# Kernel optimization log

Hardware: AMD Instinct MI355X
Metric: run time of the kernel (lower is better)

Reference implementation:

```python
import jax, jax.numpy as jnp
import numpy as np

B = 4096
INPUT_DIM = 4096
N_BLOCKS = 8
BLOCK = INPUT_DIM // N_BLOCKS  # 512
N_EXPERTS = 6
H = 1024   # expert_hidden
H2 = H // 2


def setup_inputs() -> dict:
    key = jax.random.key(0)
    ks = jax.random.split(key, 16)
    s = 0.02  # init scale keeps tanh/softmax in sane range
    return {
        "x":   jax.random.normal(ks[0], (B, INPUT_DIM), jnp.float32),
        # routers: per-block stacked weights [8, ...]
        "Wr1": jax.random.normal(ks[1], (N_BLOCKS, BLOCK, 32), jnp.float32) * s,
        "br1": jax.random.normal(ks[2], (N_BLOCKS, 32), jnp.float32) * s,
        "Wr2": jax.random.normal(ks[3], (N_BLOCKS, 32, N_EXPERTS), jnp.float32) * s,
        "br2": jax.random.normal(ks[4], (N_BLOCKS, N_EXPERTS), jnp.float32) * s,
        # experts: stacked [6, ...], shared across all 8 blocks
        "We1": jax.random.normal(ks[5], (N_EXPERTS, BLOCK, H), jnp.float32) * s,
        "be1": jax.random.normal(ks[6], (N_EXPERTS, H), jnp.float32) * s,
        "We2": jax.random.normal(ks[7], (N_EXPERTS, H, H2), jnp.float32) * s,
        "be2": jax.random.normal(ks[8], (N_EXPERTS, H2), jnp.float32) * s,
        "We3": jax.random.normal(ks[9], (N_EXPERTS, H2, 3), jnp.float32) * s,
        "be3": jax.random.normal(ks[10], (N_EXPERTS, 3), jnp.float32) * s,
        # aggregator
        "Wa1": jax.random.normal(ks[11], (3, 16), jnp.float32) * s,
        "ba1": jax.random.normal(ks[12], (16,), jnp.float32) * s,
        "Wa2": jax.random.normal(ks[13], (16, 3), jnp.float32) * s,
        "ba2": jax.random.normal(ks[14], (3,), jnp.float32) * s,
    }


def reference(x, Wr1, br1, Wr2, br2, We1, be1, We2, be2, We3, be3,
              Wa1, ba1, Wa2, ba2):
    b = x.shape[0]
    blocks = x.reshape(b, N_BLOCKS, BLOCK)                       # [b,s,d]
    # routers (one per block s)
    r1 = jax.nn.relu(jnp.einsum('bsd,sdh->bsh', blocks, Wr1) + br1)
    routing = jax.nn.softmax(
        jnp.einsum('bsh,she->bse', r1, Wr2) + br2, axis=-1)      # [b,s,E]
    # experts applied to every block (grouped GEMMs)
    h1 = jnp.tanh(jnp.einsum('bsd,edh->bseh', blocks, We1) + be1)        # [b,s,E,H]
    h2 = jnp.tanh(jnp.einsum('bseh,ehk->bsek', h1, We2) + be2)           # [b,s,E,H2]
    eo = jnp.einsum('bsek,eko->bseo', h2, We3) + be3                     # [b,s,E,3]
    weighted = jnp.einsum('bse,bseo->bso', routing, eo)                  # [b,s,3]
    final = weighted.mean(axis=1)                                        # mean over 8 blocks
    a1 = jax.nn.relu(final @ Wa1 + ba1)
    return a1 @ Wa2 + ba2                                                # [b,3]
```

## Files before the change

### kernel.cpp

```cpp
#include <hip/hip_runtime.h>
#include <cstdint>
#include <cstddef>

typedef __bf16 bf16;
typedef __bf16 bf16x4 __attribute__((ext_vector_type(4)));
typedef __bf16 bf16x8 __attribute__((ext_vector_type(8)));
typedef float  f32x4  __attribute__((ext_vector_type(4)));
typedef long long i64v;

#define NROWS   32768
#define DBLK    512
#define H1N     1024
#define H2N     512
#define NEXP    6
#define NBATCH  4096
#define HALL    (NEXP * H1N)
#define W2SCALE 32.0f
#define W2INV   0.03125f

__device__ __forceinline__ void gld16(const void* g, void* l) {
    __builtin_amdgcn_global_load_lds(
        (const __attribute__((address_space(1))) void*)g,
        (__attribute__((address_space(3))) void*)l, 16, 0, 0);
}

__device__ __forceinline__ float fast_tanh(float x) {
    float e = __expf(2.0f * x);
    return 1.0f - __fdividef(2.0f, e + 1.0f);
}

__device__ __forceinline__ float hsum16(float v) {
    v += __shfl_xor(v, 1);
    v += __shfl_xor(v, 2);
    v += __shfl_xor(v, 4);
    v += __shfl_xor(v, 8);
    return v;
}

__device__ __forceinline__ int swz(int row, int g) {
    return row * 64 + ((g ^ (row & 7)) * 8);
}
__device__ __forceinline__ int swz8(int row, int g) {
    return row * 64 + ((g ^ ((row >> 1) & 3)) << 4);
}


__global__ void cvt_bf16_kernel(const float* __restrict__ in,
                                bf16* __restrict__ out, int n4) {
    int i = blockIdx.x * blockDim.x + threadIdx.x;
    if (i >= n4) return;
    float4 v = ((const float4*)in)[i];
    bf16x4 o;
    o.x = (bf16)v.x; o.y = (bf16)v.y; o.z = (bf16)v.z; o.w = (bf16)v.w;
    ((bf16x4*)out)[i] = o;
}

__global__ __launch_bounds__(256) void transpose_cvt(
    const float* __restrict__ in, bf16* __restrict__ out, int K, int N) {
    __shared__ bf16 tile[64][66];
    int e  = blockIdx.z;
    int n0 = blockIdx.x * 64;
    int k0 = blockIdx.y * 64;
    int c  = threadIdx.x & 63;
    int rb = threadIdx.x >> 6;
    const float* src = in + (size_t)e * K * N;
    bf16* dst = out + (size_t)e * N * K;
#pragma unroll
    for (int it = 0; it < 16; ++it) {
        int k = k0 + rb + it * 4;
        int n = n0 + c;
        if (k < K && n < N) tile[rb + it * 4][c] = (bf16)src[(size_t)k * N + n];
    }
    __syncthreads();
#pragma unroll
    for (int it = 0; it < 16; ++it) {
        int n = n0 + rb + it * 4;
        int k = k0 + c;
        if (n < N && k < K) dst[(size_t)n * K + k] = tile[c][rb + it * 4];
    }
}

__global__ __launch_bounds__(256) void transpose_cvt_fp8(
    const float* __restrict__ in, uint8_t* __restrict__ out, int K, int N,
    float scale) {
    __shared__ float tile[64][65];
    int e  = blockIdx.z;
    int n0 = blockIdx.x * 64;
    int k0 = blockIdx.y * 64;
    int c  = threadIdx.x & 63;
    int rb = threadIdx.x >> 6;
    const float* src = in + (size_t)e * K * N;
    uint8_t* dst = out + (size_t)e * N * K;
#pragma unroll
    for (int it = 0; it < 16; ++it) {
        int k = k0 + rb + it * 4;
        int n = n0 + c;
        if (k < K && n < N) tile[rb + it * 4][c] = src[(size_t)k * N + n];
    }
    __syncthreads();
#pragma unroll
    for (int it = 0; it < 16; ++it) {
        int n = n0 + rb + it * 4;
        int k = k0 + c;
        if (n < N && k < K) {
            float v = tile[c][rb + it * 4] * scale;
            int p = __builtin_amdgcn_cvt_pk_fp8_f32(v, v, 0, false);
            dst[(size_t)n * K + k] = (uint8_t)(p & 0xff);
        }
    }
}

__global__ void zero_f32_kernel(float* __restrict__ p, int n) {
    int i = blockIdx.x * blockDim.x + threadIdx.x;
    if (i < n) p[i] = 0.0f;
}


__global__ __launch_bounds__(256, 2) void router_kernel(
    const bf16* __restrict__ xbf,
    const bf16* __restrict__ Wr1t,
    const float* __restrict__ br1,
    const float* __restrict__ Wr2,
    const float* __restrict__ br2,
    float* __restrict__ routing) {
    __shared__ __align__(16) bf16 sA[128 * 64];
    __shared__ __align__(16) bf16 sB[32 * 64];
    const int tid = threadIdx.x;
    const int w = tid >> 6, l = tid & 63;
    const int s  = blockIdx.y;
    const int b0 = blockIdx.x * 128;
    const int wm = w * 32;
    const int srow = l >> 3, schk = (l & 7) * 8;
    const int fr = l & 15, fq = l >> 4;
    const bf16* Ab = xbf + (size_t)s * 512;
    const bf16* Bb = Wr1t + (size_t)s * (32 * 512);

    f32x4 acc[2][2];
#pragma unroll
    for (int i = 0; i < 2; ++i)
#pragma unroll
        for (int j = 0; j < 2; ++j) acc[i][j] = (f32x4){0.f, 0.f, 0.f, 0.f};

    for (int k0 = 0; k0 < 512; k0 += 64) {
        __syncthreads();
#pragma unroll
        for (int jj = 0; jj < 4; ++jj) {
            int row = w * 32 + jj * 8;
            gld16(Ab + (size_t)(b0 + row + srow) * 4096 + k0 + schk, sA + row * 64);
        }
        gld16(Bb + (size_t)(w * 8 + srow) * 512 + k0 + schk, sB + w * 8 * 64);
        __syncthreads();
#pragma unroll
        for (int ks = 0; ks < 2; ++ks) {
            bf16x8 af[2], bfr[2];
#pragma unroll
            for (int i = 0; i < 2; ++i)
                af[i] = *(const bf16x8*)&sA[(wm + i * 16 + fr) * 64 + ks * 32 + fq * 8];
#pragma unroll
            for (int j = 0; j < 2; ++j)
                bfr[j] = *(const bf16x8*)&sB[(j * 16 + fr) * 64 + ks * 32 + fq * 8];
#pragma unroll
            for (int i = 0; i < 2; ++i)
#pragma unroll
                for (int j = 0; j < 2; ++j)
                    acc[i][j] = __builtin_amdgcn_mfma_f32_16x16x32_bf16(
                        af[i], bfr[j], acc[i][j], 0, 0, 0);
        }
    }

    float b1v[2], w2v[2][6], br2v[6];
#pragma unroll
    for (int j = 0; j < 2; ++j) {
        int col = j * 16 + fr;
        b1v[j] = br1[s * 32 + col];
#pragma unroll
        for (int e2 = 0; e2 < 6; ++e2) w2v[j][e2] = Wr2[(s * 32 + col) * 6 + e2];
    }
#pragma unroll
    for (int e2 = 0; e2 < 6; ++e2) br2v[e2] = br2[s * 6 + e2];

#pragma unroll
    for (int i = 0; i < 2; ++i) {
#pragma unroll
        for (int r = 0; r < 4; ++r) {
            float lg[6] = {0.f, 0.f, 0.f, 0.f, 0.f, 0.f};
#pragma unroll
            for (int j = 0; j < 2; ++j) {
                float t = fmaxf(acc[i][j][r] + b1v[j], 0.f);
#pragma unroll
                for (int e2 = 0; e2 < 6; ++e2) lg[e2] += t * w2v[j][e2];
            }
#pragma unroll
            for (int e2 = 0; e2 < 6; ++e2) lg[e2] = hsum16(lg[e2]) + br2v[e2];
            float mx = lg[0];
#pragma unroll
            for (int e2 = 1; e2 < 6; ++e2) mx = fmaxf(mx, lg[e2]);
            float p[6], sum = 0.f;
#pragma unroll
            for (int e2 = 0; e2 < 6; ++e2) { p[e2] = __expf(lg[e2] - mx); sum += p[e2]; }
            float inv = __fdividef(1.f, sum);
            if (fr == 0) {
                int brow = b0 + wm + i * 16 + fq * 4 + r;
                float* dst = routing + ((size_t)brow * 8 + s) * 6;
#pragma unroll
                for (int e2 = 0; e2 < 6; ++e2) dst[e2] = p[e2] * inv;
            }
        }
    }
}

__global__ __launch_bounds__(256, 4) void gemm1_kernel(
    const bf16* __restrict__ A,
    const bf16* __restrict__ B,
    const float* __restrict__ bias,
    uint8_t* __restrict__ h1,
    int ldh) {
    __shared__ __align__(16) bf16 sA[128 * 64];
    __shared__ __align__(16) bf16 sB[128 * 64];
    const int tid = threadIdx.x;
    const int w = tid >> 6, l = tid & 63;
    const int n0 = blockIdx.x * 128;
    const int m0 = blockIdx.y * 128;
    const int wm = (w & 1) * 64, wn = (w >> 1) * 64;
    const int srow = l >> 3;
    const int gcol = ((l & 7) ^ srow) * 8;
    const int fr = l & 15, fq = l >> 4;

    f32x4 acc[4][4];
#pragma unroll
    for (int i = 0; i < 4; ++i)
#pragma unroll
        for (int j = 0; j < 4; ++j) acc[i][j] = (f32x4){0.f, 0.f, 0.f, 0.f};

    for (int k0 = 0; k0 < DBLK; k0 += 64) {
        __syncthreads();
#pragma unroll
        for (int jj = 0; jj < 4; ++jj) {
            int row = w * 32 + jj * 8;
            gld16(A + (size_t)(m0 + row + srow) * DBLK + k0 + gcol, sA + row * 64);
            gld16(B + (size_t)(n0 + row + srow) * DBLK + k0 + gcol, sB + row * 64);
        }
        __syncthreads();
#pragma unroll
        for (int ks = 0; ks < 2; ++ks) {
            bf16x8 af[4], bfr[4];
#pragma unroll
            for (int i = 0; i < 4; ++i)
                af[i] = *(const bf16x8*)&sA[swz(wm + i * 16 + fr, ks * 4 + fq)];
#pragma unroll
            for (int j = 0; j < 4; ++j)
                bfr[j] = *(const bf16x8*)&sB[swz(wn + j * 16 + fr, ks * 4 + fq)];
#pragma unroll
            for (int i = 0; i < 4; ++i)
#pragma unroll
                for (int j = 0; j < 4; ++j)
                    acc[i][j] = __builtin_amdgcn_mfma_f32_16x16x32_bf16(
                        af[i], bfr[j], acc[i][j], 0, 0, 0);
        }
    }

#pragma unroll
    for (int i = 0; i < 4; ++i) {
        int colb = m0 + wm + i * 16 + fq * 4;
        float4 bb = *(const float4*)&bias[colb];
#pragma unroll
        for (int j = 0; j < 4; ++j) {
            int xrow = n0 + wn + j * 16 + fr;
            float t0 = fast_tanh(acc[i][j][0] + bb.x);
            float t1 = fast_tanh(acc[i][j][1] + bb.y);
            float t2 = fast_tanh(acc[i][j][2] + bb.z);
            float t3 = fast_tanh(acc[i][j][3] + bb.w);
            int p = 0;
            p = __builtin_amdgcn_cvt_pk_fp8_f32(t0, t1, p, false);
            p = __builtin_amdgcn_cvt_pk_fp8_f32(t2, t3, p, true);
            *(uint32_t*)&h1[(size_t)xrow * ldh + colb] = (uint32_t)p;
        }
    }
}

__global__ __launch_bounds__(256, 4) void gemm2_kernel(
    const uint8_t* __restrict__ h1,
    const uint8_t* __restrict__ W2f8t,
    const float* __restrict__ be2,
    const float* __restrict__ We3,
    float* __restrict__ eo,
    int ldh) {
    __shared__ __align__(16) uint8_t sA[128 * 64];
    __shared__ __align__(16) uint8_t sB[128 * 64];
    __shared__ float w3s[128 * 3];
    __shared__ float b2s[128];
    const int tid = threadIdx.x;
    const int w = tid >> 6, l = tid & 63;
    const int e  = blockIdx.z;
    const int n0 = blockIdx.x * 128;
    const int m0 = blockIdx.y * 128;
    const int wm = (w & 1) * 64, wn = (w >> 1) * 64;
    const int srow4 = l >> 2;
    const int g4 = (((l & 3) ^ ((l >> 3) & 3)) << 4);
    const int fr = l & 15, fq = l >> 4;
    const uint8_t* Ae = W2f8t + (size_t)e * (H2N * H1N);
    const uint8_t* Be = h1 + (size_t)e * H1N;

    if (tid < 128) {
        int c = m0 + tid;
        b2s[tid] = be2[e * H2N + c];
        w3s[tid * 3 + 0] = We3[((size_t)e * H2N + c) * 3 + 0];
        w3s[tid * 3 + 1] = We3[((size_t)e * H2N + c) * 3 + 1];
        w3s[tid * 3 + 2] = We3[((size_t)e * H2N + c) * 3 + 2];
    }

    f32x4 acc[4][4];
#pragma unroll
    for (int i = 0; i < 4; ++i)
#pragma unroll
        for (int j = 0; j < 4; ++j) acc[i][j] = (f32x4){0.f, 0.f, 0.f, 0.f};

    for (int k0 = 0; k0 < H1N; k0 += 64) {
        __syncthreads();
#pragma unroll
        for (int jj = 0; jj < 2; ++jj) {
            int row = w * 32 + jj * 16 + srow4;
            gld16(Ae + (size_t)(m0 + row) * H1N + k0 + g4, sA + (w * 32 + jj * 16) * 64);
            gld16(Be + (size_t)(n0 + row) * ldh + k0 + g4, sB + (w * 32 + jj * 16) * 64);
        }
        __syncthreads();
#pragma unroll
        for (int ks = 0; ks < 2; ++ks) {
            i64v af[4], bfr[4];
#pragma unroll
            for (int i = 0; i < 4; ++i) {
                int row = wm + i * 16 + fr;
                af[i] = *(const i64v*)&sA[swz8(row, ks * 2 + (fq >> 1)) + ((fq & 1) << 3)];
            }
#pragma unroll
            for (int j = 0; j < 4; ++j) {
                int row = wn + j * 16 + fr;
                bfr[j] = *(const i64v*)&sB[swz8(row, ks * 2 + (fq >> 1)) + ((fq & 1) << 3)];
            }
#pragma unroll
            for (int i = 0; i < 4; ++i)
#pragma unroll
                for (int j = 0; j < 4; ++j)
                    acc[i][j] = __builtin_amdgcn_mfma_f32_16x16x32_fp8_fp8(
                        af[i], bfr[j], acc[i][j], 0, 0, 0);
        }
    }

    float p[4][3];
#pragma unroll
    for (int j = 0; j < 4; ++j) { p[j][0] = 0.f; p[j][1] = 0.f; p[j][2] = 0.f; }
#pragma unroll
    for (int i = 0; i < 4; ++i) {
        int cl = wm + i * 16 + fq * 4;
        float4 bb = *(const float4*)&b2s[cl];
        float4 wa = *(const float4*)&w3s[cl * 3 + 0];
        float4 wb = *(const float4*)&w3s[cl * 3 + 4];
        float4 wc = *(const float4*)&w3s[cl * 3 + 8];
        float bias4[4] = {bb.x, bb.y, bb.z, bb.w};
        float w30[4] = {wa.x, wa.w, wb.z, wc.y};
        float w31[4] = {wa.y, wb.x, wb.w, wc.z};
        float w32[4] = {wa.z, wb.y, wc.x, wc.w};
#pragma unroll
        for (int j = 0; j < 4; ++j) {
#pragma unroll
            for (int r = 0; r < 4; ++r) {
                float t = fast_tanh(acc[i][j][r] * W2INV + bias4[r]);
                p[j][0] += t * w30[r];
                p[j][1] += t * w31[r];
                p[j][2] += t * w32[r];
            }
        }
    }
#pragma unroll
    for (int j = 0; j < 4; ++j) {
        float v0 = p[j][0], v1 = p[j][1], v2 = p[j][2];
        v0 += __shfl_xor(v0, 16); v0 += __shfl_xor(v0, 32);
        v1 += __shfl_xor(v1, 16); v1 += __shfl_xor(v1, 32);
        v2 += __shfl_xor(v2, 16); v2 += __shfl_xor(v2, 32);
        if (fq == 0) {
            int xrow = n0 + wn + j * 16 + fr;
            float* dst = eo + ((size_t)e * NROWS + xrow) * 3;
            atomicAdd(dst + 0, v0);
            atomicAdd(dst + 1, v1);
            atomicAdd(dst + 2, v2);
        }
    }
}

__global__ void final_kernel(
    const float* __restrict__ routing, const float* __restrict__ eo,
    const float* __restrict__ be3, const float* __restrict__ Wa1,
    const float* __restrict__ ba1, const float* __restrict__ Wa2,
    const float* __restrict__ ba2, float* __restrict__ out) {
    int b = blockIdx.x * blockDim.x + threadIdx.x;
    if (b >= NBATCH) return;
    float f0 = 0.f, f1 = 0.f, f2 = 0.f;
    for (int s = 0; s < 8; ++s) {
        int r = b * 8 + s;
        const float* rt = routing + (size_t)r * 6;
#pragma unroll
        for (int e = 0; e < 6; ++e) {
            float wgt = rt[e];
            const float* eop = eo + ((size_t)e * NROWS + r) * 3;
            f0 += wgt * (eop[0] + be3[e * 3 + 0]);
            f1 += wgt * (eop[1] + be3[e * 3 + 1]);
            f2 += wgt * (eop[2] + be3[e * 3 + 2]);
        }
    }
    f0 *= 0.125f; f1 *= 0.125f; f2 *= 0.125f;
    float o0 = ba2[0], o1 = ba2[1], o2 = ba2[2];
#pragma unroll
    for (int h = 0; h < 16; ++h) {
        float a = f0 * Wa1[h] + f1 * Wa1[16 + h] + f2 * Wa1[32 + h] + ba1[h];
        a = fmaxf(a, 0.f);
        o0 += a * Wa2[h * 3 + 0];
        o1 += a * Wa2[h * 3 + 1];
        o2 += a * Wa2[h * 3 + 2];
    }
    out[b * 3 + 0] = o0;
    out[b * 3 + 1] = o1;
    out[b * 3 + 2] = o2;
}


extern "C" void kernel_launch(void* const* d_in, const int* in_sizes, int n_in,
                              void* d_out, int out_size, void* d_ws, size_t ws_size,
                              hipStream_t stream) {
    const float* x   = (const float*)d_in[0];
    const float* Wr1 = (const float*)d_in[1];
    const float* br1 = (const float*)d_in[2];
    const float* Wr2 = (const float*)d_in[3];
    const float* br2 = (const float*)d_in[4];
    const float* We1 = (const float*)d_in[5];
    const float* be1 = (const float*)d_in[6];
    const float* We2 = (const float*)d_in[7];
    const float* be2 = (const float*)d_in[8];
    const float* We3 = (const float*)d_in[9];
    const float* be3 = (const float*)d_in[10];
    const float* Wa1 = (const float*)d_in[11];
    const float* ba1 = (const float*)d_in[12];
    const float* Wa2 = (const float*)d_in[13];
    const float* ba2 = (const float*)d_in[14];
    float* out = (float*)d_out;

    char* ws = (char*)d_ws;
    const size_t off_xbf  = 0;
    const size_t off_w1t  = off_xbf  + (size_t)33554432;
    const size_t off_w2t  = off_w1t  + (size_t)6291456;
    const size_t off_wr1t = off_w2t  + (size_t)6291456;
    const size_t off_rout = off_wr1t + (size_t)262144;
    const size_t off_eo   = off_rout + (size_t)786432;
    const size_t off_h1   = off_eo   + (size_t)2359296;

    if (off_h1 + (size_t)NROWS * HALL > ws_size) return;

    bf16*    xbf     = (bf16*)(ws + off_xbf);
    bf16*    W1t     = (bf16*)(ws + off_w1t);
    uint8_t* W2f8t   = (uint8_t*)(ws + off_w2t);
    bf16*    Wr1t    = (bf16*)(ws + off_wr1t);
    float*   routing = (float*)(ws + off_rout);
    float*   eo      = (float*)(ws + off_eo);
    uint8_t* h1      = (uint8_t*)(ws + off_h1);

    cvt_bf16_kernel<<<16384, 256, 0, stream>>>(x, xbf, 4194304);
    transpose_cvt<<<dim3(16, 8, 6), 256, 0, stream>>>(We1, W1t, 512, 1024);
    transpose_cvt_fp8<<<dim3(8, 16, 6), 256, 0, stream>>>(We2, W2f8t, 1024, 512, W2SCALE);
    transpose_cvt<<<dim3(1, 8, 8), 256, 0, stream>>>(Wr1, Wr1t, 512, 32);
    zero_f32_kernel<<<2304, 256, 0, stream>>>(eo, 589824);

    router_kernel<<<dim3(32, 8), 256, 0, stream>>>(xbf, Wr1t, br1, Wr2, br2, routing);

    gemm1_kernel<<<dim3(NROWS / 128, HALL / 128), 256, 0, stream>>>(
        W1t, xbf, be1, h1, HALL);
    gemm2_kernel<<<dim3(NROWS / 128, H2N / 128, NEXP), 256, 0, stream>>>(
        h1, W2f8t, be2, We3, eo, HALL);

    final_kernel<<<16, 256, 0, stream>>>(routing, eo, be3, Wa1, ba1, Wa2, ba2, out);
}
```

Measured before the change: 675.6 us.

## Enlarge gemm1 tile to 256x256 with double-buffered LDS prefetch and cheaper tanh

Reworks the first expert GEMM to use 256x256 output tiles with 512 threads, each wave computing a 128x64 sub-tile. The K loop is software-pipelined: the next 64-wide slice is loaded into a second LDS buffer while the current slice is consumed, with explicit vmcnt waits and barriers. This is meant to hide global-load latency and raise arithmetic intensity per loaded byte. It costs more LDS and registers per block, which lowers occupancy. The tanh epilogue also switches to native exp2 and rcp intrinsics.

```diff
diff --git a/kernel.cpp b/kernel.cpp
--- a/kernel.cpp
+++ b/kernel.cpp
@@ -25,8 +25,9 @@
 }
 
 __device__ __forceinline__ float fast_tanh(float x) {
-    float e = __expf(2.0f * x);
-    return 1.0f - __fdividef(2.0f, e + 1.0f);
+    float e = __builtin_amdgcn_exp2f(x * 2.8853900817779268f);
+    float r = __builtin_amdgcn_rcpf(e + 1.0f);
+    return __builtin_fmaf(-2.0f, r, 1.0f);
 }
 
 __device__ __forceinline__ float hsum16(float v) {
@@ -209,58 +210,92 @@
     }
 }
 
-__global__ __launch_bounds__(256, 4) void gemm1_kernel(
+__global__ __launch_bounds__(512, 2) void gemm1_kernel(
     const bf16* __restrict__ A,
     const bf16* __restrict__ B,
     const float* __restrict__ bias,
     uint8_t* __restrict__ h1,
     int ldh) {
-    __shared__ __align__(16) bf16 sA[128 * 64];
-    __shared__ __align__(16) bf16 sB[128 * 64];
+    __shared__ __align__(16) bf16 sA[2][256 * 64];
+    __shared__ __align__(16) bf16 sB[2][256 * 64];
     const int tid = threadIdx.x;
     const int w = tid >> 6, l = tid & 63;
-    const int n0 = blockIdx.x * 128;
-    const int m0 = blockIdx.y * 128;
-    const int wm = (w & 1) * 64, wn = (w >> 1) * 64;
+    const int n0 = blockIdx.x * 256;
+    const int m0 = blockIdx.y * 256;
+    const int wm = (w & 1) * 128;
+    const int wn = (w >> 1) * 64;
     const int srow = l >> 3;
     const int gcol = ((l & 7) ^ srow) * 8;
     const int fr = l & 15, fq = l >> 4;
 
-    f32x4 acc[4][4];
-#pragma unroll
-    for (int i = 0; i < 4; ++i)
+    f32x4 acc[8][4];
+#pragma unroll
+    for (int i = 0; i < 8; ++i)
 #pragma unroll
         for (int j = 0; j < 4; ++j) acc[i][j] = (f32x4){0.f, 0.f, 0.f, 0.f};
 
-    for (int k0 = 0; k0 < DBLK; k0 += 64) {
-        __syncthreads();
+    const bf16* Abase = A + (size_t)(m0 + w * 32 + srow) * DBLK + gcol;
+    const bf16* Bbase = B + (size_t)(n0 + w * 32 + srow) * DBLK + gcol;
+
+#pragma unroll
+    for (int jj = 0; jj < 4; ++jj) {
+        gld16(Abase + (size_t)(jj * 8) * DBLK, &sA[0][(w * 32 + jj * 8) * 64]);
+        gld16(Bbase + (size_t)(jj * 8) * DBLK, &sB[0][(w * 32 + jj * 8) * 64]);
+    }
+
+    for (int t = 0; t < 7; ++t) {
+        const int nb = (t + 1) & 1, cb = t & 1;
+        const int k1 = (t + 1) * 64;
 #pragma unroll
         for (int jj = 0; jj < 4; ++jj) {
-            int row = w * 32 + jj * 8;
-            gld16(A + (size_t)(m0 + row + srow) * DBLK + k0 + gcol, sA + row * 64);
-            gld16(B + (size_t)(n0 + row + srow) * DBLK + k0 + gcol, sB + row * 64);
-        }
-        __syncthreads();
+            gld16(Abase + (size_t)(jj * 8) * DBLK + k1, &sA[nb][(w * 32 + jj * 8) * 64]);
+            gld16(Bbase + (size_t)(jj * 8) * DBLK + k1, &sB[nb][(w * 32 + jj * 8) * 64]);
+        }
+        asm volatile("s_waitcnt vmcnt(8)" ::: "memory");
+        __builtin_amdgcn_s_barrier();
+        __builtin_amdgcn_sched_barrier(0);
 #pragma unroll
         for (int ks = 0; ks < 2; ++ks) {
-            bf16x8 af[4], bfr[4];
-#pragma unroll
-            for (int i = 0; i < 4; ++i)
-                af[i] = *(const bf16x8*)&sA[swz(wm + i * 16 + fr, ks * 4 + fq)];
+            bf16x8 af[8], bfr[4];
+#pragma unroll
+            for (int i = 0; i < 8; ++i)
+                af[i] = *(const bf16x8*)&sA[cb][swz(wm + i * 16 + fr, ks * 4 + fq)];
 #pragma unroll
             for (int j = 0; j < 4; ++j)
-                bfr[j] = *(const bf16x8*)&sB[swz(wn + j * 16 + fr, ks * 4 + fq)];
-#pragma unroll
-            for (int i = 0; i < 4; ++i)
+                bfr[j] = *(const bf16x8*)&sB[cb][swz(wn + j * 16 + fr, ks * 4 + fq)];
+#pragma unroll
+            for (int i = 0; i < 8; ++i)
 #pragma unroll
                 for (int j = 0; j < 4; ++j)
                     acc[i][j] = __builtin_amdgcn_mfma_f32_16x16x32_bf16(
                         af[i], bfr[j], acc[i][j], 0, 0, 0);
         }
-    }
-
-#pragma unroll
-    for (int i = 0; i < 4; ++i) {
+        asm volatile("" ::: "memory");
+        __builtin_amdgcn_s_barrier();
+        __builtin_amdgcn_sched_barrier(0);
+    }
+    asm volatile("s_waitcnt vmcnt(0)" ::: "memory");
+    __builtin_amdgcn_s_barrier();
+    __builtin_amdgcn_sched_barrier(0);
+#pragma unroll
+    for (int ks = 0; ks < 2; ++ks) {
+        bf16x8 af[8], bfr[4];
+#pragma unroll
+        for (int i = 0; i < 8; ++i)
+            af[i] = *(const bf16x8*)&sA[1][swz(wm + i * 16 + fr, ks * 4 + fq)];
+#pragma unroll
+        for (int j = 0; j < 4; ++j)
+            bfr[j] = *(const bf16x8*)&sB[1][swz(wn + j * 16 + fr, ks * 4 + fq)];
+#pragma unroll
+        for (int i = 0; i < 8; ++i)
+#pragma unroll
+            for (int j = 0; j < 4; ++j)
+                acc[i][j] = __builtin_amdgcn_mfma_f32_16x16x32_bf16(
+                    af[i], bfr[j], acc[i][j], 0, 0, 0);
+    }
+
+#pragma unroll
+    for (int i = 0; i < 8; ++i) {
         int colb = m0 + wm + i * 16 + fq * 4;
         float4 bb = *(const float4*)&bias[colb];
 #pragma unroll
@@ -470,7 +505,7 @@
 
     router_kernel<<<dim3(32, 8), 256, 0, stream>>>(xbf, Wr1t, br1, Wr2, br2, routing);
 
-    gemm1_kernel<<<dim3(NROWS / 128, HALL / 128), 256, 0, stream>>>(
+    gemm1_kernel<<<dim3(NROWS / 256, HALL / 256), 512, 0, stream>>>(
         W1t, xbf, be1, h1, HALL);
     gemm2_kernel<<<dim3(NROWS / 128, H2N / 128, NEXP), 256, 0, stream>>>(
         h1, W2f8t, be2, We3, eo, HALL);
```

Result: faster. 621.2 us (-8.0%).

## Restructure gemm1 into 256x256 tiles with register-staged double-buffered LDS pipeline

Applied to the files above, without the earlier changes.

Rewrites gemm1 to use 256x256 output tiles with 512 threads, where each wave computes a 128x64 block. The K loop is fully unrolled with global loads staged through registers into double-buffered LDS, and MFMA issue is raised in priority with s_setprio, so memory traffic overlaps compute. fast_tanh now uses the native exp2 and rcp builtins with an fma. The larger tile raises data reuse but doubles LDS (64KB) and increases accumulator register pressure, which may cut occupancy.

```diff
diff --git a/kernel.cpp b/kernel.cpp
--- a/kernel.cpp
+++ b/kernel.cpp
@@ -25,8 +25,9 @@
 }
 
 __device__ __forceinline__ float fast_tanh(float x) {
-    float e = __expf(2.0f * x);
-    return 1.0f - __fdividef(2.0f, e + 1.0f);
+    float e = __builtin_amdgcn_exp2f(x * 2.8853900817779268f);
+    float r = __builtin_amdgcn_rcpf(e + 1.0f);
+    return __builtin_fmaf(-2.0f, r, 1.0f);
 }
 
 __device__ __forceinline__ float hsum16(float v) {
@@ -209,71 +210,108 @@
     }
 }
 
-__global__ __launch_bounds__(256, 4) void gemm1_kernel(
+__global__ __launch_bounds__(512, 2) void gemm1_kernel(
     const bf16* __restrict__ A,
     const bf16* __restrict__ B,
     const float* __restrict__ bias,
     uint8_t* __restrict__ h1,
     int ldh) {
-    __shared__ __align__(16) bf16 sA[128 * 64];
-    __shared__ __align__(16) bf16 sB[128 * 64];
+    __shared__ __align__(16) bf16 sA[2][256 * 64];
+    __shared__ __align__(16) bf16 sB[2][256 * 64];
     const int tid = threadIdx.x;
     const int w = tid >> 6, l = tid & 63;
-    const int n0 = blockIdx.x * 128;
-    const int m0 = blockIdx.y * 128;
-    const int wm = (w & 1) * 64, wn = (w >> 1) * 64;
-    const int srow = l >> 3;
-    const int gcol = ((l & 7) ^ srow) * 8;
+    const int n0 = blockIdx.x * 256;
+    const int m0 = blockIdx.y * 256;
+    const int wm = (w & 1) * 128;
+    const int wn = (w >> 1) * 64;
     const int fr = l & 15, fq = l >> 4;
 
-    f32x4 acc[4][4];
-#pragma unroll
-    for (int i = 0; i < 4; ++i)
+    const int rbase = w * 32 + (l >> 3);
+    const int gg = l & 7;
+    const bf16* Ag = A + (size_t)(m0 + rbase) * DBLK + gg * 8;
+    const bf16* Bg = B + (size_t)(n0 + rbase) * DBLK + gg * 8;
+    const int woff = rbase * 64 + ((gg ^ (l >> 3)) * 8);
+
+    f32x4 acc[8][4];
+#pragma unroll
+    for (int i = 0; i < 8; ++i)
 #pragma unroll
         for (int j = 0; j < 4; ++j) acc[i][j] = (f32x4){0.f, 0.f, 0.f, 0.f};
 
-    for (int k0 = 0; k0 < DBLK; k0 += 64) {
-        __syncthreads();
-#pragma unroll
-        for (int jj = 0; jj < 4; ++jj) {
-            int row = w * 32 + jj * 8;
-            gld16(A + (size_t)(m0 + row + srow) * DBLK + k0 + gcol, sA + row * 64);
-            gld16(B + (size_t)(n0 + row + srow) * DBLK + k0 + gcol, sB + row * 64);
-        }
-        __syncthreads();
-#pragma unroll
-        for (int ks = 0; ks < 2; ++ks) {
-            bf16x8 af[4], bfr[4];
-#pragma unroll
-            for (int i = 0; i < 4; ++i)
-                af[i] = *(const bf16x8*)&sA[swz(wm + i * 16 + fr, ks * 4 + fq)];
-#pragma unroll
-            for (int j = 0; j < 4; ++j)
-                bfr[j] = *(const bf16x8*)&sB[swz(wn + j * 16 + fr, ks * 4 + fq)];
-#pragma unroll
-            for (int i = 0; i < 4; ++i)
-#pragma unroll
-                for (int j = 0; j < 4; ++j)
-                    acc[i][j] = __builtin_amdgcn_mfma_f32_16x16x32_bf16(
-                        af[i], bfr[j], acc[i][j], 0, 0, 0);
-        }
-    }
-
-#pragma unroll
-    for (int i = 0; i < 4; ++i) {
-        int colb = m0 + wm + i * 16 + fq * 4;
-        float4 bb = *(const float4*)&bias[colb];
-#pragma unroll
-        for (int j = 0; j < 4; ++j) {
-            int xrow = n0 + wn + j * 16 + fr;
-            float t0 = fast_tanh(acc[i][j][0] + bb.x);
-            float t1 = fast_tanh(acc[i][j][1] + bb.y);
-            float t2 = fast_tanh(acc[i][j][2] + bb.z);
-            float t3 = fast_tanh(acc[i][j][3] + bb.w);
+#define G1_LOAD(SA_, SB_, T_)                                              \
+    {                                                                      \
+        _Pragma("unroll") for (int q = 0; q < 4; ++q) {                    \
+            SA_[q] = *(const bf16x8*)(Ag + (size_t)q * 4096 + (T_) * 64);  \
+            SB_[q] = *(const bf16x8*)(Bg + (size_t)q * 4096 + (T_) * 64);  \
+        }                                                                  \
+    }
+#define G1_WRITE(SA_, SB_, BUF_)                                           \
+    {                                                                      \
+        _Pragma("unroll") for (int q = 0; q < 4; ++q) {                    \
+            *(bf16x8*)&sA[BUF_][woff + q * 512] = SA_[q];                  \
+            *(bf16x8*)&sB[BUF_][woff + q * 512] = SB_[q];                  \
+        }                                                                  \
+    }
+#define G1_COMP(BUF_)                                                      \
+    {                                                                      \
+        _Pragma("unroll") for (int ks = 0; ks < 2; ++ks) {                 \
+            bf16x8 af[8], bfr[4];                                          \
+            _Pragma("unroll") for (int i = 0; i < 8; ++i)                  \
+                af[i] = *(const bf16x8*)&sA[BUF_][swz(wm + i * 16 + fr,    \
+                                                      ks * 4 + fq)];       \
+            _Pragma("unroll") for (int j = 0; j < 4; ++j)                  \
+                bfr[j] = *(const bf16x8*)&sB[BUF_][swz(wn + j * 16 + fr,   \
+                                                       ks * 4 + fq)];      \
+            __builtin_amdgcn_s_setprio(1);                                 \
+            _Pragma("unroll") for (int i = 0; i < 8; ++i)                  \
+                _Pragma("unroll") for (int j = 0; j < 4; ++j)              \
+                    acc[i][j] = __builtin_amdgcn_mfma_f32_16x16x32_bf16(   \
+                        af[i], bfr[j], acc[i][j], 0, 0, 0);                \
+            __builtin_amdgcn_s_setprio(0);                                 \
+        }                                                                  \
+    }
+#define G1_BAR()                                                           \
+    asm volatile("s_waitcnt lgkmcnt(0)" ::: "memory");                     \
+    __builtin_amdgcn_s_barrier();                                          \
+    __builtin_amdgcn_sched_barrier(0);
+
+    bf16x8 S0A[4], S0B[4], S1A[4], S1B[4];
+    G1_LOAD(S0A, S0B, 0)
+    G1_LOAD(S1A, S1B, 1)
+    G1_WRITE(S0A, S0B, 0)
+    G1_BAR()
+    G1_LOAD(S0A, S0B, 2) G1_WRITE(S1A, S1B, 1) G1_COMP(0) G1_BAR()
+    G1_LOAD(S1A, S1B, 3) G1_WRITE(S0A, S0B, 0) G1_COMP(1) G1_BAR()
+    G1_LOAD(S0A, S0B, 4) G1_WRITE(S1A, S1B, 1) G1_COMP(0) G1_BAR()
+    G1_LOAD(S1A, S1B, 5) G1_WRITE(S0A, S0B, 0) G1_COMP(1) G1_BAR()
+    G1_LOAD(S0A, S0B, 6) G1_WRITE(S1A, S1B, 1) G1_COMP(0) G1_BAR()
+    G1_LOAD(S1A, S1B, 7) G1_WRITE(S0A, S0B, 0) G1_COMP(1) G1_BAR()
+    G1_WRITE(S1A, S1B, 1) G1_COMP(0) G1_BAR()
+    G1_COMP(1)
+
+#undef G1_LOAD
+#undef G1_WRITE
+#undef G1_COMP
+#undef G1_BAR
+
+    float4 bb[8];
+#pragma unroll
+    for (int i = 0; i < 8; ++i)
+        bb[i] = *(const float4*)&bias[m0 + wm + i * 16 + fq * 4];
+#pragma unroll
+    for (int j = 0; j < 4; ++j) {
+        int xrow = n0 + wn + j * 16 + fr;
+        uint8_t* dst = &h1[(size_t)xrow * ldh + m0 + wm + fq * 4];
+#pragma unroll
+        for (int i = 0; i < 8; ++i) {
+            float t0 = fast_tanh(acc[i][j][0] + bb[i].x);
+            float t1 = fast_tanh(acc[i][j][1] + bb[i].y);
+            float t2 = fast_tanh(acc[i][j][2] + bb[i].z);
+            float t3 = fast_tanh(acc[i][j][3] + bb[i].w);
             int p = 0;
             p = __builtin_amdgcn_cvt_pk_fp8_f32(t0, t1, p, false);
             p = __builtin_amdgcn_cvt_pk_fp8_f32(t2, t3, p, true);
-            *(uint32_t*)&h1[(size_t)xrow * ldh + colb] = (uint32_t)p;
+            *(uint32_t*)(dst + i * 16) = (uint32_t)p;
         }
     }
 }
@@ -470,7 +508,7 @@
 
     router_kernel<<<dim3(32, 8), 256, 0, stream>>>(xbf, Wr1t, br1, Wr2, br2, routing);
 
-    gemm1_kernel<<<dim3(NROWS / 128, HALL / 128), 256, 0, stream>>>(
+    gemm1_kernel<<<dim3(NROWS / 256, HALL / 256), 512, 0, stream>>>(
         W1t, xbf, be1, h1, HALL);
     gemm2_kernel<<<dim3(NROWS / 128, H2N / 128, NEXP), 256, 0, stream>>>(
         h1, W2f8t, be2, We3, eo, HALL);
```

New measurement: 661.5 us. 2.1% less time.

## Double-buffer B tile in gemm1, load A fragments directly from global

Applied to the files above, without the earlier changes.

The gemm1 kernel now double-buffers the B tile in LDS, prefetching the next k-slice while computing the current one, which removes one of the two barriers per iteration. The A operand (weights) is read straight from global memory into registers instead of being staged through LDS. fast_tanh switches to exp2 and hardware rcp intrinsics with an fma. Direct global loads for A may add latency and uncoalesced traffic that the LDS staging used to hide.

```diff
diff --git a/kernel.cpp b/kernel.cpp
--- a/kernel.cpp
+++ b/kernel.cpp
@@ -25,8 +25,9 @@
 }
 
 __device__ __forceinline__ float fast_tanh(float x) {
-    float e = __expf(2.0f * x);
-    return 1.0f - __fdividef(2.0f, e + 1.0f);
+    float e = __builtin_amdgcn_exp2f(x * 2.8853900817779268f);
+    float r = __builtin_amdgcn_rcpf(e + 1.0f);
+    return __builtin_fmaf(-2.0f, r, 1.0f);
 }
 
 __device__ __forceinline__ float hsum16(float v) {
@@ -215,65 +216,76 @@
     const float* __restrict__ bias,
     uint8_t* __restrict__ h1,
     int ldh) {
-    __shared__ __align__(16) bf16 sA[128 * 64];
-    __shared__ __align__(16) bf16 sB[128 * 64];
+    __shared__ __align__(16) bf16 sB[2][128 * 64];
     const int tid = threadIdx.x;
     const int w = tid >> 6, l = tid & 63;
     const int n0 = blockIdx.x * 128;
     const int m0 = blockIdx.y * 128;
-    const int wm = (w & 1) * 64, wn = (w >> 1) * 64;
-    const int srow = l >> 3;
-    const int gcol = ((l & 7) ^ srow) * 8;
+    const int wm = (w & 1) * 64;
+    const int wn = (w >> 1) * 64;
     const int fr = l & 15, fq = l >> 4;
 
+    const int srow = l >> 3, gg = l & 7;
+    const bf16* Bg = B + (size_t)(n0 + w * 32 + srow) * DBLK + ((gg ^ srow) * 8);
+    const bf16* Ar = A + (size_t)(m0 + wm + fr) * DBLK + fq * 8;
+
     f32x4 acc[4][4];
 #pragma unroll
     for (int i = 0; i < 4; ++i)
 #pragma unroll
         for (int j = 0; j < 4; ++j) acc[i][j] = (f32x4){0.f, 0.f, 0.f, 0.f};
 
-    for (int k0 = 0; k0 < DBLK; k0 += 64) {
-        __syncthreads();
-#pragma unroll
-        for (int jj = 0; jj < 4; ++jj) {
-            int row = w * 32 + jj * 8;
-            gld16(A + (size_t)(m0 + row + srow) * DBLK + k0 + gcol, sA + row * 64);
-            gld16(B + (size_t)(n0 + row + srow) * DBLK + k0 + gcol, sB + row * 64);
-        }
-        __syncthreads();
+#pragma unroll
+    for (int jj = 0; jj < 4; ++jj)
+        gld16(Bg + (size_t)jj * 8 * DBLK, &sB[0][(w * 32 + jj * 8) * 64]);
+    __syncthreads();
+
+#pragma unroll
+    for (int t = 0; t < 8; ++t) {
+        const int cb = t & 1;
+        if (t < 7) {
+#pragma unroll
+            for (int jj = 0; jj < 4; ++jj)
+                gld16(Bg + (size_t)jj * 8 * DBLK + (t + 1) * 64,
+                      &sB[1 - cb][(w * 32 + jj * 8) * 64]);
+        }
 #pragma unroll
         for (int ks = 0; ks < 2; ++ks) {
-            bf16x8 af[4], bfr[4];
+            bf16x8 af[4], bv[4];
 #pragma unroll
             for (int i = 0; i < 4; ++i)
-                af[i] = *(const bf16x8*)&sA[swz(wm + i * 16 + fr, ks * 4 + fq)];
+                af[i] = *(const bf16x8*)(Ar + (size_t)i * 16 * DBLK + t * 64 + ks * 32);
 #pragma unroll
             for (int j = 0; j < 4; ++j)
-                bfr[j] = *(const bf16x8*)&sB[swz(wn + j * 16 + fr, ks * 4 + fq)];
+                bv[j] = *(const bf16x8*)&sB[cb][swz(wn + j * 16 + fr, ks * 4 + fq)];
 #pragma unroll
             for (int i = 0; i < 4; ++i)
 #pragma unroll
                 for (int j = 0; j < 4; ++j)
                     acc[i][j] = __builtin_amdgcn_mfma_f32_16x16x32_bf16(
-                        af[i], bfr[j], acc[i][j], 0, 0, 0);
-        }
-    }
-
-#pragma unroll
-    for (int i = 0; i < 4; ++i) {
-        int colb = m0 + wm + i * 16 + fq * 4;
-        float4 bb = *(const float4*)&bias[colb];
-#pragma unroll
-        for (int j = 0; j < 4; ++j) {
-            int xrow = n0 + wn + j * 16 + fr;
-            float t0 = fast_tanh(acc[i][j][0] + bb.x);
-            float t1 = fast_tanh(acc[i][j][1] + bb.y);
-            float t2 = fast_tanh(acc[i][j][2] + bb.z);
-            float t3 = fast_tanh(acc[i][j][3] + bb.w);
+                        af[i], bv[j], acc[i][j], 0, 0, 0);
+        }
+        __syncthreads();
+    }
+
+    float4 bb[4];
+#pragma unroll
+    for (int i = 0; i < 4; ++i)
+        bb[i] = *(const float4*)&bias[m0 + wm + i * 16 + fq * 4];
+#pragma unroll
+    for (int j = 0; j < 4; ++j) {
+        int xrow = n0 + wn + j * 16 + fr;
+        uint8_t* dst = &h1[(size_t)xrow * ldh + m0 + wm + fq * 4];
+#pragma unroll
+        for (int i = 0; i < 4; ++i) {
+            float t0 = fast_tanh(acc[i][j][0] + bb[i].x);
+            float t1 = fast_tanh(acc[i][j][1] + bb[i].y);
+            float t2 = fast_tanh(acc[i][j][2] + bb[i].z);
+            float t3 = fast_tanh(acc[i][j][3] + bb[i].w);
             int p = 0;
             p = __builtin_amdgcn_cvt_pk_fp8_f32(t0, t1, p, false);
             p = __builtin_amdgcn_cvt_pk_fp8_f32(t2, t3, p, true);
-            *(uint32_t*)&h1[(size_t)xrow * ldh + colb] = (uint32_t)p;
+            *(uint32_t*)(dst + i * 16) = (uint32_t)p;
         }
     }
 }
```

Result: slower. 827.2 us (+22.4%).
